# Optimization experiments

Hardware: AMD Instinct MI355X
Metric: run time of the kernel (lower is better)

Reference implementation:

```python
import jax, jax.numpy as jnp
import numpy as np

B, S, D = 2, 2048, 1024
QKV = 2048
H = 16
HD = QKV // H  # 128
SCALE = HD ** -0.5


def setup_inputs() -> dict:
    key = jax.random.key(0)
    k1, k2, k3, k4, k5 = jax.random.split(key, 5)
    std = D ** -0.5
    return {
        "x": jax.random.normal(k1, (B, S, D), dtype=jnp.float32),
        "wq": jax.random.normal(k2, (QKV, D), dtype=jnp.float32) * std,
        "wk": jax.random.normal(k3, (QKV, D), dtype=jnp.float32) * std,
        "wv": jax.random.normal(k4, (QKV, D), dtype=jnp.float32) * std,
        "wo": jax.random.normal(k5, (D, QKV), dtype=jnp.float32) * (QKV ** -0.5),
    }


def reference(x, wq, wk, wv, wo):
    b, s, _ = x.shape
    # QKV projections (torch Linear: y = x @ W.T), reshape to [b, h, s, hd]
    q = (x @ wq.T).reshape(b, s, H, HD).transpose(0, 2, 1, 3)
    k = (x @ wk.T).reshape(b, s, H, HD).transpose(0, 2, 1, 3)
    v = (x @ wv.T).reshape(b, s, H, HD).transpose(0, 2, 1, 3)
    scores = jnp.einsum("bhqd,bhkd->bhqk", q, k) * SCALE
    causal = jnp.tril(jnp.ones((s, s), dtype=bool))
    scores = jnp.where(causal[None, None], scores, -jnp.inf)
    attn = jax.nn.softmax(scores, axis=-1)  # dropout p=0 (eval)
    out = jnp.einsum("bhqk,bhkd->bhqd", attn, v)
    out = out.transpose(0, 2, 1, 3).reshape(b, s, QKV)
    return out @ wo.T
```

## Files before the change

kernel.cpp:

```cpp
#include <hip/hip_runtime.h>
#include <hip/hip_bf16.h>
#include <cstdint>

#define SEQ   2048
#define DMOD  1024
#define QKVD  2048
#define NH    16
#define HDIM  128
#define NTOK  4096

typedef __bf16 bf16;
typedef bf16 bf16x4 __attribute__((ext_vector_type(4)));
typedef bf16 bf16x8 __attribute__((ext_vector_type(8)));
typedef float f32x4 __attribute__((ext_vector_type(4)));
typedef float f32x16 __attribute__((ext_vector_type(16)));
typedef uint32_t u32x4 __attribute__((ext_vector_type(4)));

typedef __attribute__((address_space(1))) void* as1_t;
typedef __attribute__((address_space(3))) void* as3_t;

__device__ __forceinline__ void gload16(const void* g, void* l) {
  __builtin_amdgcn_global_load_lds((as1_t)(uintptr_t)g, (as3_t)(uintptr_t)l, 16, 0, 0);
}

__device__ __forceinline__ uint32_t pkbf(float a, float b) {
  union { bf16 h; unsigned short u; } x, y;
  x.h = (bf16)a; y.h = (bf16)b;
  return (uint32_t)x.u | ((uint32_t)y.u << 16);
}

__device__ __forceinline__ void plswap(uint32_t& a, uint32_t& b) {
  asm("v_permlane32_swap_b32 %0, %1" : "+v"(a), "+v"(b));
}

__global__ void cast_f32_bf16(const float* __restrict__ in, bf16* __restrict__ out, int n4) {
  int i = blockIdx.x * blockDim.x + threadIdx.x;
  if (i < n4) {
    float4 v = reinterpret_cast<const float4*>(in)[i];
    bf16x4 o;
    o[0] = (bf16)v.x; o[1] = (bf16)v.y; o[2] = (bf16)v.z; o[3] = (bf16)v.w;
    reinterpret_cast<bf16x4*>(out)[i] = o;
  }
}

__global__ __launch_bounds__(512, 1) void qkv_gemm_kernel(
    const bf16* __restrict__ A, const bf16* __restrict__ Bw,
    bf16* __restrict__ Qo, bf16* __restrict__ Ko, bf16* __restrict__ Vto, float qs)
{
  __shared__ bf16 LA[2][128 * 64];
  __shared__ bf16 LB[2][256 * 64];

  const int tid  = threadIdx.x;
  const int lane = tid & 63;
  const int wid  = tid >> 6;
  const int wm   = wid >> 2;
  const int wn   = wid & 3;
  const int lm   = lane & 15;
  const int lg   = lane >> 4;

  const int g   = blockIdx.x & 7;
  const int idx = blockIdx.x >> 3;
  const int m0  = ((g & 1) * 16 + (idx & 15)) * 128;
  const int n0  = ((g >> 1) * 6 + (idx >> 4)) * 256;

  f32x4 acc[4][4];
#pragma unroll
  for (int i = 0; i < 4; ++i)
#pragma unroll
    for (int j = 0; j < 4; ++j) acc[i][j] = (f32x4)0.0f;

  auto stage = [&](int kt, int buf) {
    const int k0 = kt * 64;
    const int rl = lane >> 3;
    const int cb = (lane & 7) * 16;
#pragma unroll
    for (int i = 0; i < 2; ++i) {
      int chunk = wid * 2 + i;
      int row   = chunk * 8 + rl;
      int cx    = cb ^ ((row & 7) << 4);
      gload16(A + (size_t)(m0 + row) * DMOD + k0 + (cx >> 1), &LA[buf][chunk * 512]);
    }
#pragma unroll
    for (int i = 0; i < 4; ++i) {
      int chunk = wid * 4 + i;
      int row   = chunk * 8 + rl;
      int cx    = cb ^ ((row & 7) << 4);
      gload16(Bw + (size_t)(n0 + row) * DMOD + k0 + (cx >> 1), &LB[buf][chunk * 512]);
    }
  };

  auto rdA = [&](int buf, int mf, int kk) -> bf16x8 {
    int row = wm * 64 + mf * 16 + lm;
    int cb  = (kk * 64 + lg * 16) ^ ((row & 7) << 4);
    return *(const bf16x8*)((const char*)&LA[buf][0] + row * 128 + cb);
  };
  auto rdB = [&](int buf, int nf, int kk) -> bf16x8 {
    int row = wn * 64 + nf * 16 + lm;
    int cb  = (kk * 64 + lg * 16) ^ ((row & 7) << 4);
    return *(const bf16x8*)((const char*)&LB[buf][0] + row * 128 + cb);
  };

  stage(0, 0);

  for (int t = 0; t < 16; ++t) {
    const int c = t & 1;
    if (t < 15) {
      stage(t + 1, c ^ 1);
      asm volatile("s_waitcnt vmcnt(6)" ::: "memory");
    } else {
      asm volatile("s_waitcnt vmcnt(0)" ::: "memory");
    }
    __builtin_amdgcn_s_barrier();

    bf16x8 a[4][2], b[2][2];

#pragma unroll
    for (int mf = 0; mf < 4; ++mf)
#pragma unroll
      for (int kk = 0; kk < 2; ++kk) a[mf][kk] = rdA(c, mf, kk);
#pragma unroll
    for (int nf = 0; nf < 2; ++nf)
#pragma unroll
      for (int kk = 0; kk < 2; ++kk) b[nf][kk] = rdB(c, nf, kk);
    __builtin_amdgcn_s_barrier();
    __builtin_amdgcn_s_setprio(1);
#pragma unroll
    for (int mf = 0; mf < 4; ++mf)
#pragma unroll
      for (int nf = 0; nf < 2; ++nf)
#pragma unroll
        for (int kk = 0; kk < 2; ++kk)
          acc[mf][nf] = __builtin_amdgcn_mfma_f32_16x16x32_bf16(a[mf][kk], b[nf][kk], acc[mf][nf], 0, 0, 0);
    __builtin_amdgcn_s_setprio(0);
    __builtin_amdgcn_s_barrier();

#pragma unroll
    for (int nf = 0; nf < 2; ++nf)
#pragma unroll
      for (int kk = 0; kk < 2; ++kk) b[nf][kk] = rdB(c, 2 + nf, kk);
    __builtin_amdgcn_s_barrier();
    __builtin_amdgcn_s_setprio(1);
#pragma unroll
    for (int mf = 0; mf < 4; ++mf)
#pragma unroll
      for (int nf = 0; nf < 2; ++nf)
#pragma unroll
        for (int kk = 0; kk < 2; ++kk)
          acc[mf][2 + nf] = __builtin_amdgcn_mfma_f32_16x16x32_bf16(a[mf][kk], b[nf][kk], acc[mf][2 + nf], 0, 0, 0);
    __builtin_amdgcn_s_setprio(0);
    __builtin_amdgcn_s_barrier();
  }

#pragma unroll
  for (int mf = 0; mf < 4; ++mf) {
#pragma unroll
    for (int nf = 0; nf < 4; ++nf) {
      int row0 = m0 + wm * 64 + mf * 16 + lg * 4;
      int col  = n0 + wn * 64 + nf * 16 + lm;
      f32x4 cv = acc[mf][nf];
      if (n0 < 2048) {
#pragma unroll
        for (int r = 0; r < 4; ++r)
          Qo[(size_t)(row0 + r) * QKVD + col] = (bf16)(cv[r] * qs);
      } else if (n0 < 4096) {
        int kc = col - 2048;
#pragma unroll
        for (int r = 0; r < 4; ++r)
          Ko[(size_t)(row0 + r) * QKVD + kc] = (bf16)cv[r];
      } else {
        int vc = col - 4096;
#pragma unroll
        for (int r = 0; r < 4; ++r) {
          int tok = row0 + r; int bb = tok >> 11; int s = tok & 2047;
          Vto[((size_t)bb * QKVD + vc) * SEQ + s] = (bf16)cv[r];
        }
      }
    }
  }
}

__global__ __launch_bounds__(256, 2) void proj_kernel(
    const bf16* __restrict__ A, const bf16* __restrict__ Bw, float* __restrict__ out)
{
  __shared__ bf16 PA[2][128 * 64];
  __shared__ bf16 PB[2][64 * 64];

  const int tid  = threadIdx.x;
  const int lane = tid & 63;
  const int wid  = tid >> 6;
  const int wm   = wid >> 1;
  const int wn   = wid & 1;
  const int lm   = lane & 15;
  const int lg   = lane >> 4;

  const int g   = blockIdx.x & 7;
  const int idx = blockIdx.x >> 3;
  const int m0  = (g * 4 + (idx >> 4)) * 128;
  const int n0  = (idx & 15) * 64;

  f32x4 acc[4][2];
#pragma unroll
  for (int i = 0; i < 4; ++i)
#pragma unroll
    for (int j = 0; j < 2; ++j) acc[i][j] = (f32x4)0.0f;

  auto stage = [&](int kt, int buf) {
    const int k0 = kt * 64;
    const int rl = lane >> 3;
    const int cb = (lane & 7) * 16;
#pragma unroll
    for (int i = 0; i < 4; ++i) {
      int chunk = wid * 4 + i;
      int row   = chunk * 8 + rl;
      int cx    = cb ^ ((row & 7) << 4);
      gload16(A + (size_t)(m0 + row) * QKVD + k0 + (cx >> 1), &PA[buf][chunk * 512]);
    }
#pragma unroll
    for (int i = 0; i < 2; ++i) {
      int chunk = wid * 2 + i;
      int row   = chunk * 8 + rl;
      int cx    = cb ^ ((row & 7) << 4);
      gload16(Bw + (size_t)(n0 + row) * QKVD + k0 + (cx >> 1), &PB[buf][chunk * 512]);
    }
  };

  stage(0, 0);

  for (int t = 0; t < 32; ++t) {
    const int c = t & 1;
    if (t < 31) {
      stage(t + 1, c ^ 1);
      asm volatile("s_waitcnt vmcnt(6)" ::: "memory");
    } else {
      asm volatile("s_waitcnt vmcnt(0)" ::: "memory");
    }
    __builtin_amdgcn_s_barrier();

    bf16x8 a[4][2], b[2][2];
#pragma unroll
    for (int mf = 0; mf < 4; ++mf)
#pragma unroll
      for (int kk = 0; kk < 2; ++kk) {
        int row = wm * 64 + mf * 16 + lm;
        int cb  = (kk * 64 + lg * 16) ^ ((row & 7) << 4);
        a[mf][kk] = *(const bf16x8*)((const char*)&PA[c][0] + row * 128 + cb);
      }
#pragma unroll
    for (int nf = 0; nf < 2; ++nf)
#pragma unroll
      for (int kk = 0; kk < 2; ++kk) {
        int row = wn * 32 + nf * 16 + lm;
        int cb  = (kk * 64 + lg * 16) ^ ((row & 7) << 4);
        b[nf][kk] = *(const bf16x8*)((const char*)&PB[c][0] + row * 128 + cb);
      }
    __builtin_amdgcn_s_barrier();
#pragma unroll
    for (int mf = 0; mf < 4; ++mf)
#pragma unroll
      for (int nf = 0; nf < 2; ++nf)
#pragma unroll
        for (int kk = 0; kk < 2; ++kk)
          acc[mf][nf] = __builtin_amdgcn_mfma_f32_16x16x32_bf16(a[mf][kk], b[nf][kk], acc[mf][nf], 0, 0, 0);
    __builtin_amdgcn_s_barrier();
  }

#pragma unroll
  for (int mf = 0; mf < 4; ++mf)
#pragma unroll
    for (int nf = 0; nf < 2; ++nf) {
      int row0 = m0 + wm * 64 + mf * 16 + lg * 4;
      int col  = n0 + wn * 32 + nf * 16 + lm;
      f32x4 cv = acc[mf][nf];
#pragma unroll
      for (int r = 0; r < 4; ++r)
        out[(size_t)(row0 + r) * DMOD + col] = cv[r];
    }
}

__global__ __launch_bounds__(256, 2) void flash_kernel(
    const bf16* __restrict__ Q, const bf16* __restrict__ Kg,
    const bf16* __restrict__ Vt, bf16* __restrict__ Po, float2* __restrict__ Pml)
{
  __shared__ bf16 KV[2][16384];

  const int tid  = threadIdx.x;
  const int lane = tid & 63;
  const int wid  = tid >> 6;
  const int l31  = lane & 31;
  const int lh   = lane >> 5;

  const int id   = blockIdx.x;
  const int bh   = (id & 7) * 4 + ((id >> 3) & 3);
  const int xx   = id >> 5;
  const int pr   = xx >> 1;
  const int qpar = xx & 1;
  const int b    = bh >> 4;
  const int h    = bh & 15;

  auto stage = [&](int j, int buf) {
    bf16* kb = &KV[buf][0];
    bf16* vb = &KV[buf][8192];
    const int rb0 = wid * 16;
#pragma unroll
    for (int i = 0; i < 4; ++i) {
      int r0 = rb0 + i * 4;
      int r  = r0 + (lane >> 4);
      int c  = ((lane & 15) * 16) ^ ((r & 7) << 4);
      gload16(Kg + ((size_t)(b * SEQ + j * 64 + r)) * QKVD + h * HDIM + (c >> 1),
              kb + r0 * 128);
    }
    const int db0 = wid * 32;
#pragma unroll
    for (int i = 0; i < 4; ++i) {
      int d0 = db0 + i * 8;
      int d  = d0 + (lane >> 3);
      int c  = ((lane & 7) * 16) ^ ((d & 7) << 4);
      gload16(Vt + ((size_t)(bh * HDIM + d)) * SEQ + j * 64 + (c >> 1),
              vb + d0 * 64);
    }
  };

  for (int sub = 0; sub < 2; ++sub) {
    const int T  = sub ? (15 - pr) : pr;
    const int nu = T + 1;
    const int rA = T * 128 + wid * 32;

    bf16x8 qfr[8];
    {
      const bf16* qb = Q + ((size_t)(b * SEQ + rA + l31)) * QKVD + h * HDIM + lh * 8;
#pragma unroll
      for (int st = 0; st < 8; ++st) qfr[st] = *reinterpret_cast<const bf16x8*>(qb + st * 16);
    }

    f32x16 o[4];
#pragma unroll
    for (int c = 0; c < 4; ++c) o[c] = (f32x16)0.0f;
    float mreg = -__builtin_inff();
    float lreg = 0.0f;

    stage(qpar, 0);
    __syncthreads();

    int cur = 0;
    for (int i = 0; i < nu; ++i) {
      const int j = qpar + 2 * i;
      if (i + 1 < nu) stage(qpar + 2 * (i + 1), cur ^ 1);

      const bool act = (j * 64 <= rA + 31);
      if (act) {
        const char* kbb = (const char*)&KV[cur][0];
        const char* vbb = kbb + 16384;

        f32x16 s0 = (f32x16)0.0f, s1 = (f32x16)0.0f;
#pragma unroll
        for (int st = 0; st < 8; ++st) {
          const int r0 = l31, r1 = 32 + l31;
          bf16x8 kf0 = *(const bf16x8*)(kbb + r0 * 256 + ((lh * 16 + st * 32) ^ ((r0 & 7) << 4)));
          bf16x8 kf1 = *(const bf16x8*)(kbb + r1 * 256 + ((lh * 16 + st * 32) ^ ((r1 & 7) << 4)));
          s0 = __builtin_amdgcn_mfma_f32_32x32x16_bf16(kf0, qfr[st], s0, 0, 0, 0);
          s1 = __builtin_amdgcn_mfma_f32_32x32x16_bf16(kf1, qfr[st], s1, 0, 0, 0);
        }

        const bool full = (j * 64 + 63) <= rA;
        if (!full) {
          const int qr  = rA + l31;
          const int kb0 = j * 64 + 4 * lh;
#pragma unroll
          for (int r = 0; r < 16; ++r) {
            int key = kb0 + (r & 3) + 8 * (r >> 2);
            if (key > qr)      s0[r] = -1e30f;
            if (key + 32 > qr) s1[r] = -1e30f;
          }
        }

        float mx = s0[0];
#pragma unroll
        for (int r = 1; r < 16; ++r) mx = fmaxf(mx, s0[r]);
#pragma unroll
        for (int r = 0; r < 16; ++r) mx = fmaxf(mx, s1[r]);
        mx = fmaxf(mx, __shfl_xor(mx, 32));

        float mn;
        if (__all(mx <= mreg + 8.0f)) {
          mn = mreg;
        } else {
          mn = fmaxf(mreg, mx);
          float scl = exp2f(mreg - mn);
          mreg = mn;
          lreg *= scl;
#pragma unroll
          for (int r = 0; r < 16; ++r) {
            int row = (r & 3) + 8 * (r >> 2) + 4 * lh;
            float sr = __shfl(scl, row);
#pragma unroll
            for (int c = 0; c < 4; ++c) o[c][r] *= sr;
          }
        }

        float p[32];
#pragma unroll
        for (int r = 0; r < 16; ++r) p[r]      = exp2f(s0[r] - mn);
#pragma unroll
        for (int r = 0; r < 16; ++r) p[16 + r] = exp2f(s1[r] - mn);
        float rs = 0.0f;
#pragma unroll
        for (int r = 0; r < 32; ++r) rs += p[r];
        rs += __shfl_xor(rs, 32);
        lreg += rs;

        bf16x8 pa[4];
#pragma unroll
        for (int f = 0; f < 4; ++f) {
          const float* pp = p + f * 8;
          uint32_t w0 = pkbf(pp[0], pp[1]);
          uint32_t w1 = pkbf(pp[2], pp[3]);
          uint32_t w2 = pkbf(pp[4], pp[5]);
          uint32_t w3 = pkbf(pp[6], pp[7]);
          plswap(w0, w2);
          plswap(w1, w3);
          u32x4 w = {w0, w1, w2, w3};
          pa[f] = __builtin_bit_cast(bf16x8, w);
        }

#pragma unroll
        for (int c = 0; c < 4; ++c) {
          const int d = c * 32 + l31;
          const char* vrow = vbb + d * 128;
          const int dx = (d & 7) << 4;
#pragma unroll
          for (int f = 0; f < 4; ++f) {
            bf16x8 vf = *(const bf16x8*)(vrow + ((f * 32 + lh * 16) ^ dx));
            o[c] = __builtin_amdgcn_mfma_f32_32x32x16_bf16(pa[f], vf, o[c], 0, 0, 0);
          }
        }
      }

      __syncthreads();
      cur ^= 1;
    }

    const int part = (bh * 16 + T) * 2 + qpar;
#pragma unroll
    for (int c = 0; c < 4; ++c)
#pragma unroll
      for (int r = 0; r < 16; ++r) {
        int row = (r & 3) + 8 * (r >> 2) + 4 * lh;
        Po[((size_t)part * 128 + wid * 32 + row) * 128 + c * 32 + l31] = (bf16)o[c][r];
      }
    if (lane < 32)
      Pml[part * 128 + wid * 32 + lane] = make_float2(mreg, lreg);
  }
}

__global__ void merge_kernel(const bf16* __restrict__ Po, const float2* __restrict__ Pml,
                             bf16* __restrict__ Ob)
{
  const int id  = blockIdx.x;
  const int bh  = id >> 4;
  const int t   = id & 15;
  const int tid = threadIdx.x;
  const int row = tid >> 1;
  const int dh  = (tid & 1) * 64;
  const int p0  = id * 2, p1 = id * 2 + 1;

  float2 ml0 = Pml[p0 * 128 + row];
  float2 ml1 = Pml[p1 * 128 + row];
  float M  = fmaxf(ml0.x, ml1.x);
  float w0 = exp2f(ml0.x - M);
  float w1 = exp2f(ml1.x - M);
  float inv = 1.0f / (ml0.y * w0 + ml1.y * w1);
  w0 *= inv; w1 *= inv;

  const bf16* o0 = Po + ((size_t)p0 * 128 + row) * 128 + dh;
  const bf16* o1 = Po + ((size_t)p1 * 128 + row) * 128 + dh;
  const int b = bh >> 4, h = bh & 15;
  bf16* out = Ob + ((size_t)(b * SEQ + t * 128 + row)) * QKVD + h * HDIM + dh;

#pragma unroll
  for (int v = 0; v < 8; ++v) {
    bf16x8 a = reinterpret_cast<const bf16x8*>(o0)[v];
    bf16x8 c = reinterpret_cast<const bf16x8*>(o1)[v];
    bf16x8 w;
#pragma unroll
    for (int k = 0; k < 8; ++k) w[k] = (bf16)((float)a[k] * w0 + (float)c[k] * w1);
    reinterpret_cast<bf16x8*>(out)[v] = w;
  }
}

extern "C" void kernel_launch(void* const* d_in, const int* in_sizes, int n_in,
                              void* d_out, int out_size, void* d_ws, size_t ws_size,
                              hipStream_t stream) {
  const float* x  = (const float*)d_in[0];
  const float* wq = (const float*)d_in[1];
  const float* wk = (const float*)d_in[2];
  const float* wv = (const float*)d_in[3];
  const float* wo = (const float*)d_in[4];
  float* out = (float*)d_out;

  bf16* xb  = (bf16*)d_ws;
  bf16* wqb = xb  + (size_t)NTOK * DMOD;
  bf16* wkb = wqb + (size_t)QKVD * DMOD;
  bf16* wvb = wkb + (size_t)QKVD * DMOD;
  bf16* wob = wvb + (size_t)QKVD * DMOD;
  bf16* Qb  = wob + (size_t)DMOD * QKVD;
  bf16* Kb  = Qb  + (size_t)NTOK * QKVD;
  bf16* Vtb = Kb  + (size_t)NTOK * QKVD;
  bf16* Ob  = Vtb + (size_t)NTOK * QKVD;
  bf16* Po  = Ob  + (size_t)NTOK * QKVD;
  float2* Pml = (float2*)(Po + (size_t)1024 * 128 * 128);

  cast_f32_bf16<<<(NTOK * DMOD / 4) / 256, 256, 0, stream>>>(x,  xb,  NTOK * DMOD / 4);
  cast_f32_bf16<<<(QKVD * DMOD / 4) / 256, 256, 0, stream>>>(wq, wqb, QKVD * DMOD / 4);
  cast_f32_bf16<<<(QKVD * DMOD / 4) / 256, 256, 0, stream>>>(wk, wkb, QKVD * DMOD / 4);
  cast_f32_bf16<<<(QKVD * DMOD / 4) / 256, 256, 0, stream>>>(wv, wvb, QKVD * DMOD / 4);
  cast_f32_bf16<<<(DMOD * QKVD / 4) / 256, 256, 0, stream>>>(wo, wob, DMOD * QKVD / 4);

  const float qs = 0.08838834764831845f * 1.4426950408889634f;
  qkv_gemm_kernel<<<768, 512, 0, stream>>>(xb, wqb, Qb, Kb, Vtb, qs);

  flash_kernel<<<512, 256, 0, stream>>>(Qb, Kb, Vtb, Po, Pml);
  merge_kernel<<<512, 256, 0, stream>>>(Po, Pml, Ob);

  proj_kernel<<<512, 256, 0, stream>>>(Ob, wob, out);
}
```

Baseline: 190.4 us.

## Triple-buffer GEMM pipelines, enlarge proj tiles, fuse weight casts, widen K swizzle

Both GEMMs move from double-buffered LDS to a three-slot ring with prefetch depth two and matching vmcnt waits. The QKV block mapping is reordered. The output projection switches to 128x128 tiles with setprio-bracketed MFMA phases at one block per CU. The four weight casts are merged into one launch, and the flash kernel's K tile swizzle widens from 8 to 16 rows to cut LDS bank conflicts. The deeper pipeline raises LDS use and lowers occupancy, and the proj grid halves to 256 blocks.

```diff
diff --git a/kernel.cpp b/kernel.cpp
--- a/kernel.cpp
+++ b/kernel.cpp
@@ -43,12 +43,23 @@
   }
 }
 
+__global__ void cast_w4(const float* __restrict__ p0, const float* __restrict__ p1,
+                        const float* __restrict__ p2, const float* __restrict__ p3,
+                        bf16* __restrict__ out) {
+  int i = blockIdx.x * blockDim.x + threadIdx.x;
+  const float* src = (i < 524288) ? p0 : (i < 1048576) ? p1 : (i < 1572864) ? p2 : p3;
+  int off = i & 524287;
+  float4 v = reinterpret_cast<const float4*>(src)[off];
+  bf16x4 o;
+  o[0] = (bf16)v.x; o[1] = (bf16)v.y; o[2] = (bf16)v.z; o[3] = (bf16)v.w;
+  reinterpret_cast<bf16x4*>(out)[i] = o;
+}
+
 __global__ __launch_bounds__(512, 1) void qkv_gemm_kernel(
     const bf16* __restrict__ A, const bf16* __restrict__ Bw,
     bf16* __restrict__ Qo, bf16* __restrict__ Ko, bf16* __restrict__ Vto, float qs)
 {
-  __shared__ bf16 LA[2][128 * 64];
-  __shared__ bf16 LB[2][256 * 64];
+  __shared__ bf16 RING[3][24576];
 
   const int tid  = threadIdx.x;
   const int lane = tid & 63;
@@ -60,8 +71,8 @@
 
   const int g   = blockIdx.x & 7;
   const int idx = blockIdx.x >> 3;
-  const int m0  = ((g & 1) * 16 + (idx & 15)) * 128;
-  const int n0  = ((g >> 1) * 6 + (idx >> 4)) * 256;
+  const int n0  = (g * 3 + (idx >> 5)) * 256;
+  const int m0  = (idx & 31) * 128;
 
   f32x4 acc[4][4];
 #pragma unroll
@@ -69,59 +80,57 @@
 #pragma unroll
     for (int j = 0; j < 4; ++j) acc[i][j] = (f32x4)0.0f;
 
-  auto stage = [&](int kt, int buf) {
+  auto stage = [&](int kt, int slot) {
     const int k0 = kt * 64;
+    char* Ab = (char*)&RING[slot][0];
+    char* Bb = Ab + 16384;
     const int rl = lane >> 3;
     const int cb = (lane & 7) * 16;
 #pragma unroll
-    for (int i = 0; i < 2; ++i) {
-      int chunk = wid * 2 + i;
+    for (int r2 = 0; r2 < 2; ++r2) {
+      int chunk = r2 * 8 + wid;
       int row   = chunk * 8 + rl;
       int cx    = cb ^ ((row & 7) << 4);
-      gload16(A + (size_t)(m0 + row) * DMOD + k0 + (cx >> 1), &LA[buf][chunk * 512]);
-    }
-#pragma unroll
-    for (int i = 0; i < 4; ++i) {
-      int chunk = wid * 4 + i;
+      gload16(A + (size_t)(m0 + row) * DMOD + k0 + (cx >> 1), Ab + chunk * 1024);
+    }
+#pragma unroll
+    for (int r2 = 0; r2 < 4; ++r2) {
+      int chunk = r2 * 8 + wid;
       int row   = chunk * 8 + rl;
       int cx    = cb ^ ((row & 7) << 4);
-      gload16(Bw + (size_t)(n0 + row) * DMOD + k0 + (cx >> 1), &LB[buf][chunk * 512]);
+      gload16(Bw + (size_t)(n0 + row) * DMOD + k0 + (cx >> 1), Bb + chunk * 1024);
     }
   };
 
-  auto rdA = [&](int buf, int mf, int kk) -> bf16x8 {
-    int row = wm * 64 + mf * 16 + lm;
-    int cb  = (kk * 64 + lg * 16) ^ ((row & 7) << 4);
-    return *(const bf16x8*)((const char*)&LA[buf][0] + row * 128 + cb);
-  };
-  auto rdB = [&](int buf, int nf, int kk) -> bf16x8 {
-    int row = wn * 64 + nf * 16 + lm;
-    int cb  = (kk * 64 + lg * 16) ^ ((row & 7) << 4);
-    return *(const bf16x8*)((const char*)&LB[buf][0] + row * 128 + cb);
-  };
-
-  stage(0, 0);
-
+  stage(0, 0); stage(1, 1); stage(2, 2);
+
+  int cur = 0;
   for (int t = 0; t < 16; ++t) {
-    const int c = t & 1;
-    if (t < 15) {
-      stage(t + 1, c ^ 1);
-      asm volatile("s_waitcnt vmcnt(6)" ::: "memory");
-    } else {
-      asm volatile("s_waitcnt vmcnt(0)" ::: "memory");
-    }
-    __builtin_amdgcn_s_barrier();
+    if (t <= 13)      asm volatile("s_waitcnt vmcnt(12)" ::: "memory");
+    else if (t == 14) asm volatile("s_waitcnt vmcnt(6)"  ::: "memory");
+    else              asm volatile("s_waitcnt vmcnt(0)"  ::: "memory");
+    __builtin_amdgcn_s_barrier();
+
+    const char* Ab = (const char*)&RING[cur][0];
+    const char* Bb = Ab + 16384;
 
     bf16x8 a[4][2], b[2][2];
-
 #pragma unroll
     for (int mf = 0; mf < 4; ++mf)
 #pragma unroll
-      for (int kk = 0; kk < 2; ++kk) a[mf][kk] = rdA(c, mf, kk);
+      for (int kk = 0; kk < 2; ++kk) {
+        int row = wm * 64 + mf * 16 + lm;
+        int cx  = (kk * 64 + lg * 16) ^ ((row & 7) << 4);
+        a[mf][kk] = *(const bf16x8*)(Ab + row * 128 + cx);
+      }
 #pragma unroll
     for (int nf = 0; nf < 2; ++nf)
 #pragma unroll
-      for (int kk = 0; kk < 2; ++kk) b[nf][kk] = rdB(c, nf, kk);
+      for (int kk = 0; kk < 2; ++kk) {
+        int row = wn * 64 + nf * 16 + lm;
+        int cx  = (kk * 64 + lg * 16) ^ ((row & 7) << 4);
+        b[nf][kk] = *(const bf16x8*)(Bb + row * 128 + cx);
+      }
     __builtin_amdgcn_s_barrier();
     __builtin_amdgcn_s_setprio(1);
 #pragma unroll
@@ -137,7 +146,11 @@
 #pragma unroll
     for (int nf = 0; nf < 2; ++nf)
 #pragma unroll
-      for (int kk = 0; kk < 2; ++kk) b[nf][kk] = rdB(c, 2 + nf, kk);
+      for (int kk = 0; kk < 2; ++kk) {
+        int row = wn * 64 + (2 + nf) * 16 + lm;
+        int cx  = (kk * 64 + lg * 16) ^ ((row & 7) << 4);
+        b[nf][kk] = *(const bf16x8*)(Bb + row * 128 + cx);
+      }
     __builtin_amdgcn_s_barrier();
     __builtin_amdgcn_s_setprio(1);
 #pragma unroll
@@ -149,6 +162,9 @@
           acc[mf][2 + nf] = __builtin_amdgcn_mfma_f32_16x16x32_bf16(a[mf][kk], b[nf][kk], acc[mf][2 + nf], 0, 0, 0);
     __builtin_amdgcn_s_setprio(0);
     __builtin_amdgcn_s_barrier();
+
+    if (t + 3 < 16) stage(t + 3, cur);
+    cur = (cur == 2) ? 0 : cur + 1;
   }
 
 #pragma unroll
@@ -179,11 +195,10 @@
   }
 }
 
-__global__ __launch_bounds__(256, 2) void proj_kernel(
+__global__ __launch_bounds__(256, 1) void proj_kernel(
     const bf16* __restrict__ A, const bf16* __restrict__ Bw, float* __restrict__ out)
 {
-  __shared__ bf16 PA[2][128 * 64];
-  __shared__ bf16 PB[2][64 * 64];
+  __shared__ bf16 RING[3][16384];
 
   const int tid  = threadIdx.x;
   const int lane = tid & 63;
@@ -194,47 +209,49 @@
   const int lg   = lane >> 4;
 
   const int g   = blockIdx.x & 7;
-  const int idx = blockIdx.x >> 3;
-  const int m0  = (g * 4 + (idx >> 4)) * 128;
-  const int n0  = (idx & 15) * 64;
-
-  f32x4 acc[4][2];
+  const int mb  = blockIdx.x >> 3;
+  const int n0  = g * 128;
+  const int m0  = mb * 128;
+
+  f32x4 acc[4][4];
 #pragma unroll
   for (int i = 0; i < 4; ++i)
 #pragma unroll
-    for (int j = 0; j < 2; ++j) acc[i][j] = (f32x4)0.0f;
-
-  auto stage = [&](int kt, int buf) {
+    for (int j = 0; j < 4; ++j) acc[i][j] = (f32x4)0.0f;
+
+  auto stage = [&](int kt, int slot) {
     const int k0 = kt * 64;
+    char* Ab = (char*)&RING[slot][0];
+    char* Bb = Ab + 16384;
     const int rl = lane >> 3;
     const int cb = (lane & 7) * 16;
 #pragma unroll
-    for (int i = 0; i < 4; ++i) {
-      int chunk = wid * 4 + i;
+    for (int r2 = 0; r2 < 4; ++r2) {
+      int chunk = r2 * 4 + wid;
       int row   = chunk * 8 + rl;
       int cx    = cb ^ ((row & 7) << 4);
-      gload16(A + (size_t)(m0 + row) * QKVD + k0 + (cx >> 1), &PA[buf][chunk * 512]);
-    }
-#pragma unroll
-    for (int i = 0; i < 2; ++i) {
-      int chunk = wid * 2 + i;
+      gload16(A + (size_t)(m0 + row) * QKVD + k0 + (cx >> 1), Ab + chunk * 1024);
+    }
+#pragma unroll
+    for (int r2 = 0; r2 < 4; ++r2) {
+      int chunk = r2 * 4 + wid;
       int row   = chunk * 8 + rl;
       int cx    = cb ^ ((row & 7) << 4);
-      gload16(Bw + (size_t)(n0 + row) * QKVD + k0 + (cx >> 1), &PB[buf][chunk * 512]);
+      gload16(Bw + (size_t)(n0 + row) * QKVD + k0 + (cx >> 1), Bb + chunk * 1024);
     }
   };
 
-  stage(0, 0);
-
+  stage(0, 0); stage(1, 1); stage(2, 2);
+
+  int cur = 0;
   for (int t = 0; t < 32; ++t) {
-    const int c = t & 1;
-    if (t < 31) {
-      stage(t + 1, c ^ 1);
-      asm volatile("s_waitcnt vmcnt(6)" ::: "memory");
-    } else {
-      asm volatile("s_waitcnt vmcnt(0)" ::: "memory");
-    }
-    __builtin_amdgcn_s_barrier();
+    if (t <= 29)      asm volatile("s_waitcnt vmcnt(16)" ::: "memory");
+    else if (t == 30) asm volatile("s_waitcnt vmcnt(8)"  ::: "memory");
+    else              asm volatile("s_waitcnt vmcnt(0)"  ::: "memory");
+    __builtin_amdgcn_s_barrier();
+
+    const char* Ab = (const char*)&RING[cur][0];
+    const char* Bb = Ab + 16384;
 
     bf16x8 a[4][2], b[2][2];
 #pragma unroll
@@ -242,18 +259,19 @@
 #pragma unroll
       for (int kk = 0; kk < 2; ++kk) {
         int row = wm * 64 + mf * 16 + lm;
-        int cb  = (kk * 64 + lg * 16) ^ ((row & 7) << 4);
-        a[mf][kk] = *(const bf16x8*)((const char*)&PA[c][0] + row * 128 + cb);
+        int cx  = (kk * 64 + lg * 16) ^ ((row & 7) << 4);
+        a[mf][kk] = *(const bf16x8*)(Ab + row * 128 + cx);
       }
 #pragma unroll
     for (int nf = 0; nf < 2; ++nf)
 #pragma unroll
       for (int kk = 0; kk < 2; ++kk) {
-        int row = wn * 32 + nf * 16 + lm;
-        int cb  = (kk * 64 + lg * 16) ^ ((row & 7) << 4);
-        b[nf][kk] = *(const bf16x8*)((const char*)&PB[c][0] + row * 128 + cb);
-      }
-    __builtin_amdgcn_s_barrier();
+        int row = wn * 64 + nf * 16 + lm;
+        int cx  = (kk * 64 + lg * 16) ^ ((row & 7) << 4);
+        b[nf][kk] = *(const bf16x8*)(Bb + row * 128 + cx);
+      }
+    __builtin_amdgcn_s_barrier();
+    __builtin_amdgcn_s_setprio(1);
 #pragma unroll
     for (int mf = 0; mf < 4; ++mf)
 #pragma unroll
@@ -261,15 +279,39 @@
 #pragma unroll
         for (int kk = 0; kk < 2; ++kk)
           acc[mf][nf] = __builtin_amdgcn_mfma_f32_16x16x32_bf16(a[mf][kk], b[nf][kk], acc[mf][nf], 0, 0, 0);
-    __builtin_amdgcn_s_barrier();
+    __builtin_amdgcn_s_setprio(0);
+    __builtin_amdgcn_s_barrier();
+
+#pragma unroll
+    for (int nf = 0; nf < 2; ++nf)
+#pragma unroll
+      for (int kk = 0; kk < 2; ++kk) {
+        int row = wn * 64 + (2 + nf) * 16 + lm;
+        int cx  = (kk * 64 + lg * 16) ^ ((row & 7) << 4);
+        b[nf][kk] = *(const bf16x8*)(Bb + row * 128 + cx);
+      }
+    __builtin_amdgcn_s_barrier();
+    __builtin_amdgcn_s_setprio(1);
+#pragma unroll
+    for (int mf = 0; mf < 4; ++mf)
+#pragma unroll
+      for (int nf = 0; nf < 2; ++nf)
+#pragma unroll
+        for (int kk = 0; kk < 2; ++kk)
+          acc[mf][2 + nf] = __builtin_amdgcn_mfma_f32_16x16x32_bf16(a[mf][kk], b[nf][kk], acc[mf][2 + nf], 0, 0, 0);
+    __builtin_amdgcn_s_setprio(0);
+    __builtin_amdgcn_s_barrier();
+
+    if (t + 3 < 32) stage(t + 3, cur);
+    cur = (cur == 2) ? 0 : cur + 1;
   }
 
 #pragma unroll
   for (int mf = 0; mf < 4; ++mf)
 #pragma unroll
-    for (int nf = 0; nf < 2; ++nf) {
+    for (int nf = 0; nf < 4; ++nf) {
       int row0 = m0 + wm * 64 + mf * 16 + lg * 4;
-      int col  = n0 + wn * 32 + nf * 16 + lm;
+      int col  = n0 + wn * 64 + nf * 16 + lm;
       f32x4 cv = acc[mf][nf];
 #pragma unroll
       for (int r = 0; r < 4; ++r)
@@ -305,7 +347,7 @@
     for (int i = 0; i < 4; ++i) {
       int r0 = rb0 + i * 4;
       int r  = r0 + (lane >> 4);
-      int c  = ((lane & 15) * 16) ^ ((r & 7) << 4);
+      int c  = ((lane & 15) * 16) ^ ((r & 15) << 4);
       gload16(Kg + ((size_t)(b * SEQ + j * 64 + r)) * QKVD + h * HDIM + (c >> 1),
               kb + r0 * 128);
     }
@@ -355,8 +397,8 @@
 #pragma unroll
         for (int st = 0; st < 8; ++st) {
           const int r0 = l31, r1 = 32 + l31;
-          bf16x8 kf0 = *(const bf16x8*)(kbb + r0 * 256 + ((lh * 16 + st * 32) ^ ((r0 & 7) << 4)));
-          bf16x8 kf1 = *(const bf16x8*)(kbb + r1 * 256 + ((lh * 16 + st * 32) ^ ((r1 & 7) << 4)));
+          bf16x8 kf0 = *(const bf16x8*)(kbb + r0 * 256 + ((lh * 16 + st * 32) ^ ((r0 & 15) << 4)));
+          bf16x8 kf1 = *(const bf16x8*)(kbb + r1 * 256 + ((lh * 16 + st * 32) ^ ((r1 & 15) << 4)));
           s0 = __builtin_amdgcn_mfma_f32_32x32x16_bf16(kf0, qfr[st], s0, 0, 0, 0);
           s1 = __builtin_amdgcn_mfma_f32_32x32x16_bf16(kf1, qfr[st], s1, 0, 0, 0);
         }
@@ -499,9 +541,7 @@
 
   bf16* xb  = (bf16*)d_ws;
   bf16* wqb = xb  + (size_t)NTOK * DMOD;
-  bf16* wkb = wqb + (size_t)QKVD * DMOD;
-  bf16* wvb = wkb + (size_t)QKVD * DMOD;
-  bf16* wob = wvb + (size_t)QKVD * DMOD;
+  bf16* wob = wqb + (size_t)3 * QKVD * DMOD;
   bf16* Qb  = wob + (size_t)DMOD * QKVD;
   bf16* Kb  = Qb  + (size_t)NTOK * QKVD;
   bf16* Vtb = Kb  + (size_t)NTOK * QKVD;
@@ -509,11 +549,8 @@
   bf16* Po  = Ob  + (size_t)NTOK * QKVD;
   float2* Pml = (float2*)(Po + (size_t)1024 * 128 * 128);
 
-  cast_f32_bf16<<<(NTOK * DMOD / 4) / 256, 256, 0, stream>>>(x,  xb,  NTOK * DMOD / 4);
-  cast_f32_bf16<<<(QKVD * DMOD / 4) / 256, 256, 0, stream>>>(wq, wqb, QKVD * DMOD / 4);
-  cast_f32_bf16<<<(QKVD * DMOD / 4) / 256, 256, 0, stream>>>(wk, wkb, QKVD * DMOD / 4);
-  cast_f32_bf16<<<(QKVD * DMOD / 4) / 256, 256, 0, stream>>>(wv, wvb, QKVD * DMOD / 4);
-  cast_f32_bf16<<<(DMOD * QKVD / 4) / 256, 256, 0, stream>>>(wo, wob, DMOD * QKVD / 4);
+  cast_f32_bf16<<<(NTOK * DMOD / 4) / 256, 256, 0, stream>>>(x, xb, NTOK * DMOD / 4);
+  cast_w4<<<8192, 256, 0, stream>>>(wq, wk, wv, wo, wqb);
 
   const float qs = 0.08838834764831845f * 1.4426950408889634f;
   qkv_gemm_kernel<<<768, 512, 0, stream>>>(xb, wqb, Qb, Kb, Vtb, qs);
@@ -521,5 +558,5 @@
   flash_kernel<<<512, 256, 0, stream>>>(Qb, Kb, Vtb, Po, Pml);
   merge_kernel<<<512, 256, 0, stream>>>(Po, Pml, Ob);
 
-  proj_kernel<<<512, 256, 0, stream>>>(Ob, wob, out);
-}
+  proj_kernel<<<256, 256, 0, stream>>>(Ob, wob, out);
+}
```

Result: no change. 192.3 us (+1.0%).
